# Performance work log

Measured on AMD Instinct MI355X. Metric: run time of the kernel, lower is better.

## Reference

```python
import jax, jax.numpy as jnp
from jax import lax
import numpy as np

B = 64          # batch
HW = 28         # image height/width (hardcoded in module)
LATENT = 256    # latent_size
LABEL = 10      # label_size
FEAT = 64 * HW * HW  # 50176, encoder/decoder fc feature dim


def _conv(x, w, pad):
    # x: [N,C,H,W], w: [O,I,kH,kW]
    return lax.conv_general_dilated(
        x, w, (1, 1), ((pad, pad), (pad, pad)),
        dimension_numbers=('NCHW', 'OIHW', 'NCHW'))


def _conv_transpose(x, w, b, pad):
    # ConvTranspose2d(stride=1, padding=pad) == conv with flipped, transposed
    # kernel and padding k-1-pad. w: [I,O,kH,kW] (torch ConvTranspose layout).
    k = w.shape[2]
    wt = jnp.flip(w, (2, 3)).transpose(1, 0, 2, 3)  # [O,I,kH,kW]
    return _conv(x, wt, k - 1 - pad) + b[None, :, None, None]


def _encoder(images, c1w, c1b, c2w, c2b, fcw, fcb):
    x = jax.nn.relu(_conv(images, c1w, 2) + c1b[None, :, None, None])
    x = jax.nn.relu(_conv(x, c2w, 2) + c2b[None, :, None, None])
    x = x.reshape(x.shape[0], FEAT)
    return jnp.tanh(x @ fcw.T + fcb)


def _decoder(z, fcw, fcb, ct2w, ct2b, ct1w, ct1b):
    x = jnp.arctanh(z)
    x = (x @ fcw.T + fcb).reshape(-1, 64, HW, HW)
    x = jax.nn.relu(_conv_transpose(x, ct2w, ct2b, 2))
    return _conv_transpose(x, ct1w, ct1b, 2)


def _hopfield_weight(patterns):
    # TrainHopfield: Hebbian outer-product sum with mean subtraction,
    # zero diagonal, normalized by number of patterns. One GEMM.
    rho = jnp.mean(patterns)
    t = patterns - rho                      # [L, latent]
    w = t.T @ t                             # [latent, latent]
    w = w - jnp.diag(jnp.diag(w))
    return w / patterns.shape[0]


def _cluster(s0, w):
    # Batched version of: iterate s = sign(w @ s) up to LATENT steps,
    # stopping per-sample when energy -s@w@s stops changing.
    def energy(s):
        return -jnp.einsum('bi,ij,bj->b', s, w, s)

    def step(carry, _):
        s, prev_e, done = carry
        new_s = jnp.sign(s @ w.T)           # w symmetric; per-sample w@s
        e = energy(new_s)
        s_next = jnp.where(done[:, None], s, new_s)
        prev_e_next = jnp.where(done, prev_e, e)
        done_next = done | (e == prev_e)
        return (s_next, prev_e_next, done_next), None

    init = (s0, energy(s0), jnp.zeros(s0.shape[0], dtype=bool))
    (s, _, _), _ = lax.scan(step, init, None, length=LATENT)
    return s


def setup_inputs() -> dict:
    key = jax.random.key(0)
    ks = jax.random.split(key, 12)
    s = 0.05
    f32 = jnp.float32
    return {
        'images': jax.random.normal(ks[0], (B, 1, HW, HW), f32),
        'enc_c1_w': jax.random.normal(ks[1], (32, 1, 5, 5), f32) * s,
        'enc_c1_b': jnp.zeros((32,), f32),
        'enc_c2_w': jax.random.normal(ks[2], (64, 32, 5, 5), f32) * s,
        'enc_c2_b': jnp.zeros((64,), f32),
        'enc_fc_w': jax.random.normal(ks[3], (LATENT, FEAT), f32) * 0.005,
        'enc_fc_b': jnp.zeros((LATENT,), f32),
        'dec_fc_w': jax.random.normal(ks[4], (FEAT, LATENT), f32) * s,
        'dec_fc_b': jnp.zeros((FEAT,), f32),
        'dec_ct2_w': jax.random.normal(ks[5], (64, 32, 5, 5), f32) * s,
        'dec_ct2_b': jnp.zeros((32,), f32),
        'dec_ct1_w': jax.random.normal(ks[6], (32, 1, 5, 5), f32) * s,
        'dec_ct1_b': jnp.zeros((1,), f32),
        'sm_w': jax.random.normal(ks[7], (LABEL, LATENT), f32) * s,
        'sm_b': jnp.zeros((LABEL,), f32),
        'label_latent': jnp.tanh(jax.random.normal(ks[8], (LABEL, LATENT), f32)),
    }


def reference(images, enc_c1_w, enc_c1_b, enc_c2_w, enc_c2_b, enc_fc_w,
              enc_fc_b, dec_fc_w, dec_fc_b, dec_ct2_w, dec_ct2_b, dec_ct1_w,
              dec_ct1_b, sm_w, sm_b, label_latent):
    z = _encoder(images, enc_c1_w, enc_c1_b, enc_c2_w, enc_c2_b,
                 enc_fc_w, enc_fc_b)                       # [B, latent]
    w = _hopfield_weight(jnp.sign(label_latent))           # [latent, latent]
    s0 = lax.stop_gradient(jnp.sign(z))                    # detached copy
    clustered = _cluster(s0, w)                            # [B, latent]
    cluster_probs = jax.nn.softmax(clustered @ label_latent.T, axis=1)
    class_probs = jax.nn.softmax(z @ sm_w.T + sm_b, axis=1)
    recon = _decoder(z, dec_fc_w, dec_fc_b, dec_ct2_w, dec_ct2_b,
                     dec_ct1_w, dec_ct1_b)                 # [B,1,28,28]
    return (cluster_probs, class_probs, recon)
```

## Files before the change

### kernel.cpp

```cpp
#include <hip/hip_runtime.h>
#include <hip/hip_bf16.h>
#include <math.h>

#define BATCH 64
#define HW 28
#define PIX 784
#define LATENT 256
#define LABEL 10
#define FEAT 50176
#define KS 28
#define KCH 1792
#define TSTR 36

typedef __attribute__((ext_vector_type(8))) short bf16x8;
typedef __attribute__((ext_vector_type(4))) float f32x4;

__device__ __forceinline__ float sgnf(float v) {
    return (v > 0.f) ? 1.f : ((v < 0.f) ? -1.f : 0.f);
}

__device__ __forceinline__ short f2bf(float f) {
    union { float f; unsigned u; } v; v.f = f;
    unsigned r = v.u + 0x7FFF + ((v.u >> 16) & 1);
    return (short)(r >> 16);
}
__device__ __forceinline__ float bf2f(short s) {
    union { unsigned u; float f; } v; v.u = ((unsigned)(unsigned short)s) << 16;
    return v.f;
}

template<int G, int FLIP>
__global__ __launch_bounds__(256) void conv5_k(const float* __restrict__ in,
                        const float* __restrict__ w,
                        const float* __restrict__ bias, float* __restrict__ out,
                        int IC, int OC, int relu) {
    int b = blockIdx.x, oc0 = blockIdx.y * G;
    __shared__ float plp[2][32 * TSTR];
    int tid = threadIdx.x;

    for (int t = tid; t < 2 * 32 * TSTR; t += 256) ((float*)plp)[t] = 0.f;

    bool actS = tid < 196;
    int ys = tid / 7, qs = tid % 7;

    int q = tid & 7, yy = tid >> 3;
    bool actC = (q < 7) && (yy < 28);
    int x0 = q * 4;

    float acc[G][4];
    #pragma unroll
    for (int g = 0; g < G; ++g)
        #pragma unroll
        for (int xi = 0; xi < 4; ++xi) acc[g][xi] = 0.f;

    __syncthreads();
    if (actS) {
        float4 v = *(const float4*)&in[((size_t)(b * IC + 0)) * PIX + tid * 4];
        *(float2*)&plp[0][(ys + 2) * TSTR + 4 * qs + 2] = make_float2(v.x, v.y);
        *(float2*)&plp[0][(ys + 2) * TSTR + 4 * qs + 4] = make_float2(v.z, v.w);
    }
    __syncthreads();

    for (int ic = 0; ic < IC; ++ic) {
        float4 vn;
        bool more = (ic + 1) < IC;
        if (more && actS)
            vn = *(const float4*)&in[((size_t)(b * IC + ic + 1)) * PIX + tid * 4];

        const float* tile = plp[ic & 1];
        if (actC) {
            #pragma unroll
            for (int dy = 0; dy < 5; ++dy) {
                float4 ra = *(const float4*)&tile[(yy + dy) * TSTR + x0];
                float4 rb = *(const float4*)&tile[(yy + dy) * TSTR + x0 + 4];
                float rw[8] = {ra.x, ra.y, ra.z, ra.w, rb.x, rb.y, rb.z, rb.w};
                #pragma unroll
                for (int g = 0; g < G; ++g) {
                    #pragma unroll
                    for (int dx = 0; dx < 5; ++dx) {
                        float wv = FLIP
                            ? w[((size_t)ic * OC + (oc0 + g)) * 25 + (4 - dy) * 5 + (4 - dx)]
                            : w[((size_t)(oc0 + g) * IC + ic) * 25 + dy * 5 + dx];
                        #pragma unroll
                        for (int xi = 0; xi < 4; ++xi)
                            acc[g][xi] += rw[xi + dx] * wv;
                    }
                }
            }
        }
        if (more && actS) {
            float* nt = plp[(ic + 1) & 1];
            *(float2*)&nt[(ys + 2) * TSTR + 4 * qs + 2] = make_float2(vn.x, vn.y);
            *(float2*)&nt[(ys + 2) * TSTR + 4 * qs + 4] = make_float2(vn.z, vn.w);
        }
        __syncthreads();
    }

    if (actC) {
        #pragma unroll
        for (int g = 0; g < G; ++g) {
            float bv = bias[oc0 + g];
            float4 o;
            o.x = acc[g][0] + bv;
            o.y = acc[g][1] + bv;
            o.z = acc[g][2] + bv;
            o.w = acc[g][3] + bv;
            if (relu) {
                o.x = fmaxf(o.x, 0.f); o.y = fmaxf(o.y, 0.f);
                o.z = fmaxf(o.z, 0.f); o.w = fmaxf(o.w, 0.f);
            }
            *(float4*)&out[((size_t)(b * OC + (oc0 + g))) * PIX + yy * HW + x0] = o;
        }
    }
}

__global__ __launch_bounds__(64) void c2_mfma_k(const short* __restrict__ xh,
                        const short* __restrict__ xm, const short* __restrict__ xl,
                        const short* __restrict__ wb,
                        const float* __restrict__ bias, float* __restrict__ out) {
    int b = blockIdx.x;
    int t0 = blockIdx.y * 4;
    int lane = threadIdx.x;
    int prow = lane & 15, kgrp = lane >> 4;

    f32x4 acc[4][4];
    #pragma unroll
    for (int pt = 0; pt < 4; ++pt)
        #pragma unroll
        for (int nt = 0; nt < 4; ++nt) acc[pt][nt] = (f32x4){0.f, 0.f, 0.f, 0.f};

    int py[4], px[4];
    bool ptv[4];
    #pragma unroll
    for (int pt = 0; pt < 4; ++pt) {
        int p = (t0 + pt) * 16 + prow;
        ptv[pt] = (t0 + pt) < 49;
        py[pt] = p / 28; px[pt] = p % 28;
    }

    for (int tap = 0; tap < 25; ++tap) {
        int dy = tap / 5 - 2, dx = tap % 5 - 2;
        const short* wt = wb + (size_t)tap * 2048;
        bf16x8 B0[4], B1[4], B2[4];
        #pragma unroll
        for (int nt = 0; nt < 4; ++nt) {
            int off = (nt * 16 + prow) * 32 + kgrp * 8;
            B0[nt] = *(const bf16x8*)&wt[off];
            B1[nt] = *(const bf16x8*)&wt[51200 + off];
            B2[nt] = *(const bf16x8*)&wt[102400 + off];
        }
        #pragma unroll
        for (int pt = 0; pt < 4; ++pt) {
            int ysrc = py[pt] + dy, xsrc = px[pt] + dx;
            bool valid = ptv[pt] && (ysrc >= 0) && (ysrc < 28) && (xsrc >= 0) && (xsrc < 28);
            bf16x8 ah = {0,0,0,0,0,0,0,0}, am = {0,0,0,0,0,0,0,0}, al = {0,0,0,0,0,0,0,0};
            if (valid) {
                size_t o = ((size_t)b * PIX + ysrc * 28 + xsrc) * 32 + kgrp * 8;
                ah = *(const bf16x8*)&xh[o];
                am = *(const bf16x8*)&xm[o];
                al = *(const bf16x8*)&xl[o];
            }
            #pragma unroll
            for (int nt = 0; nt < 4; ++nt) {
                acc[pt][nt] = __builtin_amdgcn_mfma_f32_16x16x32_bf16(ah, B0[nt], acc[pt][nt], 0, 0, 0);
                acc[pt][nt] = __builtin_amdgcn_mfma_f32_16x16x32_bf16(ah, B1[nt], acc[pt][nt], 0, 0, 0);
                acc[pt][nt] = __builtin_amdgcn_mfma_f32_16x16x32_bf16(am, B0[nt], acc[pt][nt], 0, 0, 0);
                acc[pt][nt] = __builtin_amdgcn_mfma_f32_16x16x32_bf16(ah, B2[nt], acc[pt][nt], 0, 0, 0);
                acc[pt][nt] = __builtin_amdgcn_mfma_f32_16x16x32_bf16(am, B1[nt], acc[pt][nt], 0, 0, 0);
                acc[pt][nt] = __builtin_amdgcn_mfma_f32_16x16x32_bf16(al, B0[nt], acc[pt][nt], 0, 0, 0);
            }
        }
    }

    __shared__ float ot[64][17];
    float bv = bias[lane];
    for (int pt = 0; pt < 4; ++pt) {
        if (!ptv[pt]) continue;
        #pragma unroll
        for (int nt = 0; nt < 4; ++nt)
            #pragma unroll
            for (int r = 0; r < 4; ++r)
                ot[nt * 16 + prow][kgrp * 4 + r] = acc[pt][nt][r];
        float* op = &out[((size_t)(b * 64 + lane)) * PIX + (t0 + pt) * 16];
        #pragma unroll
        for (int i = 0; i < 4; ++i) {
            float4 o;
            o.x = fmaxf(ot[lane][i * 4 + 0] + bv, 0.f);
            o.y = fmaxf(ot[lane][i * 4 + 1] + bv, 0.f);
            o.z = fmaxf(ot[lane][i * 4 + 2] + bv, 0.f);
            o.w = fmaxf(ot[lane][i * 4 + 3] + bv, 0.f);
            *(float4*)&op[i * 4] = o;
        }
    }
}

__global__ void xsplit3_k(const float* __restrict__ x, short* __restrict__ xh,
                          short* __restrict__ xm, short* __restrict__ xl) {
    __shared__ float lds[32][17];
    int b = blockIdx.x, pbase = blockIdx.y * 16;
    int t = threadIdx.x;
    if (t < 128) {
        int ic = t >> 2, pj = (t & 3) * 4;
        float4 v = *(const float4*)&x[((size_t)(b * 32 + ic)) * PIX + pbase + pj];
        lds[ic][pj + 0] = v.x; lds[ic][pj + 1] = v.y;
        lds[ic][pj + 2] = v.z; lds[ic][pj + 3] = v.w;
    }
    __syncthreads();
    int p = t >> 4, ic2 = (t & 15) * 2;
    size_t o = ((size_t)b * PIX + pbase + p) * 32 + ic2;
    short2 h, m, l;
    {
        float v = lds[ic2][p];
        short s0 = f2bf(v); float r = v - bf2f(s0);
        short s1 = f2bf(r); float r2 = r - bf2f(s1);
        h.x = s0; m.x = s1; l.x = f2bf(r2);
    }
    {
        float v = lds[ic2 + 1][p];
        short s0 = f2bf(v); float r = v - bf2f(s0);
        short s1 = f2bf(r); float r2 = r - bf2f(s1);
        h.y = s0; m.y = s1; l.y = f2bf(r2);
    }
    *(short2*)&xh[o] = h;
    *(short2*)&xm[o] = m;
    *(short2*)&xl[o] = l;
}

__global__ void wprep3_k(const float* __restrict__ w, short* __restrict__ wb) {
    int j = blockIdx.x * 256 + threadIdx.x;
    if (j < 51200) {
        int ic = j & 31;
        int oc = (j >> 5) & 63;
        int tap = j >> 11;
        float v = w[((size_t)oc * 32 + ic) * 25 + tap];
        short s0 = f2bf(v); float r = v - bf2f(s0);
        short s1 = f2bf(r); float r2 = r - bf2f(s1);
        wb[j] = s0;
        wb[51200 + j] = s1;
        wb[102400 + j] = f2bf(r2);
    }
}

__global__ __launch_bounds__(64) void ct2_mfma_k(const short* __restrict__ xb,
                        const short* __restrict__ wb,
                        const float* __restrict__ bias, float* __restrict__ out) {
    int b = blockIdx.x;
    int pbase = blockIdx.y * 16;
    int lane = threadIdx.x;
    int prow = lane & 15;
    int kgrp = lane >> 4;
    int p = pbase + prow;
    int py = p / 28, px = p % 28;

    f32x4 acc0 = {0.f, 0.f, 0.f, 0.f};
    f32x4 acc1 = {0.f, 0.f, 0.f, 0.f};

    for (int tap = 0; tap < 25; ++tap) {
        int dy = tap / 5 - 2, dx = tap % 5 - 2;
        int ysrc = py + dy, xsrc = px + dx;
        bool valid = (ysrc >= 0) && (ysrc < 28) && (xsrc >= 0) && (xsrc < 28);
        int ps = ysrc * 28 + xsrc;

        bf16x8 a0 = {0,0,0,0,0,0,0,0}, a1 = {0,0,0,0,0,0,0,0};
        if (valid) {
            const bf16x8* ap = (const bf16x8*)&xb[((size_t)b * PIX + ps) * 64 + kgrp * 8];
            a0 = ap[0];
            a1 = ap[4];
        }
        const short* wt = &wb[(size_t)tap * 32 * 64];
        int oc_l = lane & 15;
        bf16x8 b00 = *(const bf16x8*)&wt[oc_l * 64 + kgrp * 8];
        bf16x8 b01 = *(const bf16x8*)&wt[oc_l * 64 + 32 + kgrp * 8];
        bf16x8 b10 = *(const bf16x8*)&wt[(16 + oc_l) * 64 + kgrp * 8];
        bf16x8 b11 = *(const bf16x8*)&wt[(16 + oc_l) * 64 + 32 + kgrp * 8];

        acc0 = __builtin_amdgcn_mfma_f32_16x16x32_bf16(a0, b00, acc0, 0, 0, 0);
        acc0 = __builtin_amdgcn_mfma_f32_16x16x32_bf16(a1, b01, acc0, 0, 0, 0);
        acc1 = __builtin_amdgcn_mfma_f32_16x16x32_bf16(a0, b10, acc1, 0, 0, 0);
        acc1 = __builtin_amdgcn_mfma_f32_16x16x32_bf16(a1, b11, acc1, 0, 0, 0);
    }

    __shared__ float ot[32][16];
    int drow = (lane >> 4) * 4;
    #pragma unroll
    for (int r = 0; r < 4; ++r) {
        ot[lane & 15][drow + r]        = acc0[r];
        ot[16 + (lane & 15)][drow + r] = acc1[r];
    }
    __syncthreads();
    int oc = lane >> 1, ph = (lane & 1) * 8;
    float bv = bias[oc];
    float4 o0, o1;
    o0.x = fmaxf(ot[oc][ph + 0] + bv, 0.f);
    o0.y = fmaxf(ot[oc][ph + 1] + bv, 0.f);
    o0.z = fmaxf(ot[oc][ph + 2] + bv, 0.f);
    o0.w = fmaxf(ot[oc][ph + 3] + bv, 0.f);
    o1.x = fmaxf(ot[oc][ph + 4] + bv, 0.f);
    o1.y = fmaxf(ot[oc][ph + 5] + bv, 0.f);
    o1.z = fmaxf(ot[oc][ph + 6] + bv, 0.f);
    o1.w = fmaxf(ot[oc][ph + 7] + bv, 0.f);
    float* op = &out[((size_t)(b * 32 + oc)) * PIX + pbase + ph];
    *(float4*)&op[0] = o0;
    *(float4*)&op[4] = o1;
}

__global__ void wprep_k(const float* __restrict__ w, short* __restrict__ wb) {
    int j = blockIdx.x * 256 + threadIdx.x;
    if (j < 25 * 32 * 64) {
        int ic = j & 63;
        int oc = (j >> 6) & 31;
        int tap = j >> 11;
        int dyi = tap / 5, dxi = tap % 5;
        wb[j] = f2bf(w[((size_t)ic * 32 + oc) * 25 + (4 - dyi) * 5 + (4 - dxi)]);
    }
}

__global__ void xpose16_k(const short* __restrict__ y16, short* __restrict__ xb) {
    __shared__ short lds[64][16];
    int b = blockIdx.x, pbase = blockIdx.y * 16;
    int t = threadIdx.x;
    {
        int ic = t >> 2, pj = (t & 3) * 4;
        short4 v = *(const short4*)&y16[((size_t)(b * 64 + ic)) * PIX + pbase + pj];
        lds[ic][pj + 0] = v.x;
        lds[ic][pj + 1] = v.y;
        lds[ic][pj + 2] = v.z;
        lds[ic][pj + 3] = v.w;
    }
    __syncthreads();
    {
        int p = t >> 4, icq = (t & 15) * 4;
        short4 s;
        s.x = lds[icq + 0][p];
        s.y = lds[icq + 1][p];
        s.z = lds[icq + 2][p];
        s.w = lds[icq + 3][p];
        *(short4*)&xb[((size_t)b * PIX + pbase + p) * 64 + icq] = s;
    }
}

__global__ void enc_fc_part_k(const float* __restrict__ x, const float* __restrict__ w,
                              float* __restrict__ part) {
    int n0 = blockIdx.x * 4;
    int ks = blockIdx.y;
    int kl = threadIdx.x & 31;
    int mi = threadIdx.x >> 5;

    float acc[8][4];
    #pragma unroll
    for (int mg = 0; mg < 8; ++mg)
        #pragma unroll
        for (int nt = 0; nt < 4; ++nt) acc[mg][nt] = 0.f;

    int kend = (ks + 1) * KCH;
    for (int kk = ks * KCH + kl * 4; kk < kend; kk += 128) {
        float4 xv[8];
        #pragma unroll
        for (int mg = 0; mg < 8; ++mg)
            xv[mg] = *(const float4*)&x[(size_t)(mg * 8 + mi) * FEAT + kk];
        #pragma unroll
        for (int nt = 0; nt < 4; ++nt) {
            float4 wv = *(const float4*)&w[(size_t)(n0 + nt) * FEAT + kk];
            #pragma unroll
            for (int mg = 0; mg < 8; ++mg) {
                acc[mg][nt] += xv[mg].x * wv.x + xv[mg].y * wv.y
                             + xv[mg].z * wv.z + xv[mg].w * wv.w;
            }
        }
    }

    #pragma unroll
    for (int mg = 0; mg < 8; ++mg) {
        #pragma unroll
        for (int nt = 0; nt < 4; ++nt) {
            float v = acc[mg][nt];
            v += __shfl_xor(v, 16, 64);
            v += __shfl_xor(v, 8, 64);
            v += __shfl_xor(v, 4, 64);
            v += __shfl_xor(v, 2, 64);
            v += __shfl_xor(v, 1, 64);
            if (kl == 0)
                part[(ks * BATCH + (mg * 8 + mi)) * LATENT + (n0 + nt)] = v;
        }
    }
}

__global__ void enc_fc_fin_k(const float* __restrict__ part, const float* __restrict__ bias,
                             float* __restrict__ z, short* __restrict__ xah,
                             short* __restrict__ xam) {
    int m = blockIdx.x;
    int n = threadIdx.x;
    int idx = m * 256 + n;
    float a = bias[n];
    for (int ksi = 0; ksi < KS; ++ksi) a += part[ksi * BATCH * LATENT + idx];
    float zv = tanhf(a);
    z[idx] = zv;
    float xv = atanhf(zv);
    short h = f2bf(xv);
    xah[idx] = h;
    xam[idx] = f2bf(xv - bf2f(h));
}

__global__ void hop_rho_k(const float* __restrict__ ll, float* __restrict__ rho_out) {
    float p = 0.f;
    for (int t = threadIdx.x; t < LABEL * LATENT; t += 256) p += sgnf(ll[t]);
    __shared__ float red[8];
    for (int o = 32; o; o >>= 1) p += __shfl_down(p, o, 64);
    if ((threadIdx.x & 63) == 0) red[threadIdx.x >> 6] = p;
    __syncthreads();
    if (threadIdx.x == 0)
        rho_out[0] = (red[0] + red[1] + red[2] + red[3]) / (float)(LABEL * LATENT);
}

__global__ void hop_w_k(const float* __restrict__ ll, const float* __restrict__ rho_p,
                        float* __restrict__ wout) {
    int i = blockIdx.x, j = threadIdx.x;
    float rho = rho_p[0];
    float acc = 0.f;
    #pragma unroll
    for (int l = 0; l < LABEL; ++l) {
        float a = sgnf(ll[l * LATENT + i]) - rho;
        float b = sgnf(ll[l * LATENT + j]) - rho;
        acc += a * b;
    }
    wout[i * LATENT + j] = (i == j) ? 0.f : acc / 10.f;
}

__global__ __launch_bounds__(1024) void cluster_k(const float* __restrict__ z,
                          const float* __restrict__ w,
                          const float* __restrict__ ll, float* __restrict__ out) {
    int b = blockIdx.x;
    int t = threadIdx.x;
    int i = t & 255;
    int q = t >> 8;
    int lane = t & 63;
    int wvid = t >> 6;

    __shared__ float s_sh[LATENT];
    __shared__ float part[1024];
    __shared__ float red[4];
    __shared__ float cflag[4];
    __shared__ int ctl_sh;
    __shared__ float logit[LABEL];

    float wreg[64];
    #pragma unroll
    for (int jj = 0; jj < 64; ++jj)
        wreg[jj] = w[(q * 64 + jj) * LATENT + i];

    float s_cur = 0.f, s_old = 2.f, v = 0.f;
    float e_prev = 0.f;
    if (q == 0) {
        s_cur = sgnf(z[b * LATENT + i]);
        s_sh[i] = s_cur;
    }
    __syncthreads();

    {
        float p0 = 0.f, p1 = 0.f;
        #pragma unroll
        for (int jj = 0; jj < 64; jj += 2) {
            p0 += wreg[jj]     * s_sh[q * 64 + jj];
            p1 += wreg[jj + 1] * s_sh[q * 64 + jj + 1];
        }
        part[t] = p0 + p1;
    }
    __syncthreads();
    if (q == 0) {
        v = part[i] + part[i + 256] + part[i + 512] + part[i + 768];
        float p = s_cur * v;
        #pragma unroll
        for (int o = 32; o; o >>= 1) p += __shfl_down(p, o, 64);
        if (lane == 0) red[wvid] = p;
    }
    __syncthreads();
    if (t == 0) e_prev = -(red[0] + red[1] + red[2] + red[3]);

    for (int it = 0; it < LATENT; ++it) {
        if (q == 0) {
            float ns = sgnf(v);
            unsigned long long m = __ballot(ns == s_old);
            if (lane == 0) cflag[wvid] = (m == ~0ull) ? 1.f : 0.f;
            s_sh[i] = ns;
            s_old = s_cur;
            s_cur = ns;
        }
        __syncthreads();
        {
            float p0 = 0.f, p1 = 0.f;
            #pragma unroll
            for (int jj = 0; jj < 64; jj += 2) {
                p0 += wreg[jj]     * s_sh[q * 64 + jj];
                p1 += wreg[jj + 1] * s_sh[q * 64 + jj + 1];
            }
            part[t] = p0 + p1;
        }
        __syncthreads();
        if (q == 0) {
            v = part[i] + part[i + 256] + part[i + 512] + part[i + 768];
            float p = s_cur * v;
            #pragma unroll
            for (int o = 32; o; o >>= 1) p += __shfl_down(p, o, 64);
            if (lane == 0) red[wvid] = p;
        }
        __syncthreads();
        if (t == 0) {
            float e = -(red[0] + red[1] + red[2] + red[3]);
            int c = 0;
            if (e == e_prev) c = 1;
            else if (it >= 1 && cflag[0] != 0.f && cflag[1] != 0.f &&
                     cflag[2] != 0.f && cflag[3] != 0.f)
                c = (((LATENT - 1 - it) & 1) == 0) ? 2 : 3;
            else e_prev = e;
            ctl_sh = c;
        }
        __syncthreads();
        int c = ctl_sh;
        if (c != 0) {
            if (c == 3 && q == 0) s_sh[i] = s_old;
            break;
        }
    }
    __syncthreads();

    if (wvid < LABEL) {
        float p = 0.f;
        #pragma unroll
        for (int r = 0; r < 4; ++r)
            p += s_sh[r * 64 + lane] * ll[wvid * LATENT + r * 64 + lane];
        #pragma unroll
        for (int o = 32; o; o >>= 1) p += __shfl_down(p, o, 64);
        if (lane == 0) logit[wvid] = p;
    }
    __syncthreads();
    if (t == 0) {
        float mx = logit[0];
        for (int c = 1; c < LABEL; ++c) mx = fmaxf(mx, logit[c]);
        float ex[LABEL];
        float s = 0.f;
        for (int c = 0; c < LABEL; ++c) { ex[c] = expf(logit[c] - mx); s += ex[c]; }
        for (int c = 0; c < LABEL; ++c) out[b * LABEL + c] = ex[c] / s;
    }
}

__device__ __forceinline__ float block_sum256(float p, float* red) {
    __syncthreads();
    for (int o = 32; o; o >>= 1) p += __shfl_down(p, o, 64);
    if ((threadIdx.x & 63) == 0) red[threadIdx.x >> 6] = p;
    __syncthreads();
    return red[0] + red[1] + red[2] + red[3];
}

__global__ void class_k(const float* __restrict__ z, const float* __restrict__ smw,
                        const float* __restrict__ smb, float* __restrict__ out) {
    int b = blockIdx.x;
    int i = threadIdx.x;
    __shared__ float red[8];
    __shared__ float logit[LABEL];
    float zi = z[b * LATENT + i];
    for (int c = 0; c < LABEL; ++c) {
        float p = zi * smw[c * LATENT + i];
        float t = block_sum256(p, red);
        if (i == 0) logit[c] = t + smb[c];
    }
    __syncthreads();
    if (i == 0) {
        float mx = logit[0];
        for (int c = 1; c < LABEL; ++c) mx = fmaxf(mx, logit[c]);
        float ex[LABEL];
        float s = 0.f;
        for (int c = 0; c < LABEL; ++c) { ex[c] = expf(logit[c] - mx); s += ex[c]; }
        for (int c = 0; c < LABEL; ++c) out[b * LABEL + c] = ex[c] / s;
    }
}

__global__ __launch_bounds__(256) void dec_fc_mfma_k(const short* __restrict__ xah,
                         const short* __restrict__ xam,
                         const float* __restrict__ w,
                         const float* __restrict__ bias, short* __restrict__ y16) {
    int tid = threadIdx.x;
    int lane = tid & 63, wv = tid >> 6;
    int prow = lane & 15, kgrp = lane >> 4;
    int n0 = blockIdx.x * 64;
    int nb = n0 + wv * 16;

    f32x4 acc[4];
    #pragma unroll
    for (int mi = 0; mi < 4; ++mi) acc[mi] = (f32x4){0.f, 0.f, 0.f, 0.f};

    for (int kc = 0; kc < 8; ++kc) {
        int kof = kc * 32 + kgrp * 8;
        const float* wp = &w[(size_t)(nb + prow) * LATENT + kof];
        float4 w0 = *(const float4*)&wp[0];
        float4 w1 = *(const float4*)&wp[4];
        bf16x8 bf;
        bf[0] = f2bf(w0.x); bf[1] = f2bf(w0.y); bf[2] = f2bf(w0.z); bf[3] = f2bf(w0.w);
        bf[4] = f2bf(w1.x); bf[5] = f2bf(w1.y); bf[6] = f2bf(w1.z); bf[7] = f2bf(w1.w);
        #pragma unroll
        for (int mi = 0; mi < 4; ++mi) {
            bf16x8 ah = *(const bf16x8*)&xah[(mi * 16 + prow) * LATENT + kof];
            bf16x8 am = *(const bf16x8*)&xam[(mi * 16 + prow) * LATENT + kof];
            acc[mi] = __builtin_amdgcn_mfma_f32_16x16x32_bf16(ah, bf, acc[mi], 0, 0, 0);
            acc[mi] = __builtin_amdgcn_mfma_f32_16x16x32_bf16(am, bf, acc[mi], 0, 0, 0);
        }
    }

    __shared__ short ot[64 * 72];
    float bv = bias[nb + prow];
    #pragma unroll
    for (int mi = 0; mi < 4; ++mi)
        #pragma unroll
        for (int r = 0; r < 4; ++r) {
            int m = mi * 16 + kgrp * 4 + r;
            ot[m * 72 + wv * 16 + prow] = f2bf(acc[mi][r] + bv);
        }
    __syncthreads();
    int m = tid >> 2, q = tid & 3;
    #pragma unroll
    for (int i = 0; i < 2; ++i) {
        *(int4*)&y16[(size_t)m * FEAT + n0 + i * 32 + q * 8] =
            *(int4*)&ot[m * 72 + i * 32 + q * 8];
    }
}

extern "C" void kernel_launch(void* const* d_in, const int* in_sizes, int n_in,
                              void* d_out, int out_size, void* d_ws, size_t ws_size,
                              hipStream_t stream) {
    const float* images   = (const float*)d_in[0];
    const float* c1w      = (const float*)d_in[1];
    const float* c1b      = (const float*)d_in[2];
    const float* c2w      = (const float*)d_in[3];
    const float* c2b      = (const float*)d_in[4];
    const float* efw      = (const float*)d_in[5];
    const float* efb      = (const float*)d_in[6];
    const float* dfw      = (const float*)d_in[7];
    const float* dfb      = (const float*)d_in[8];
    const float* ct2w     = (const float*)d_in[9];
    const float* ct2b     = (const float*)d_in[10];
    const float* ct1w     = (const float*)d_in[11];
    const float* ct1b     = (const float*)d_in[12];
    const float* smw      = (const float*)d_in[13];
    const float* smb      = (const float*)d_in[14];
    const float* ll       = (const float*)d_in[15];

    float* out = (float*)d_out;
    float* ws  = (float*)d_ws;

    float* big0 = ws;
    float* big1 = ws + 3211264;
    float* part = ws + 3211264 + 1605632;
    float* z    = part + KS * BATCH * LATENT;
    float* whop = z + BATCH * LATENT;
    float* rho  = whop + LATENT * LATENT;
    float* xsa  = rho + 4;
    short* xah  = (short*)xsa;
    short* xam  = xah + 16384;
    short* xbf  = (short*)(xsa + 16384);
    short* wbf  = (short*)(xsa + 16384 + 1605632);
    short* xh3  = xbf;
    short* xm3  = xbf + 1605632;
    short* xl3  = (short*)(xsa + 16384 + 1605632 + 25600);
    short* wb3  = xl3 + 1605632;
    short* y16  = (short*)big0;

    conv5_k<4,0><<<dim3(BATCH, 8), 256, 0, stream>>>(images, c1w, c1b, big1, 1, 32, 1);
    wprep3_k<<<200, 256, 0, stream>>>(c2w, wb3);
    xsplit3_k<<<dim3(BATCH, 49), 256, 0, stream>>>(big1, xh3, xm3, xl3);
    c2_mfma_k<<<dim3(BATCH, 13), 64, 0, stream>>>(xh3, xm3, xl3, wb3, c2b, big0);
    enc_fc_part_k<<<dim3(64, KS), 256, 0, stream>>>(big0, efw, part);
    enc_fc_fin_k<<<BATCH, 256, 0, stream>>>(part, efb, z, xah, xam);

    hop_rho_k<<<1, 256, 0, stream>>>(ll, rho);
    hop_w_k<<<LATENT, 256, 0, stream>>>(ll, rho, whop);
    cluster_k<<<BATCH, 1024, 0, stream>>>(z, whop, ll, out);
    class_k<<<BATCH, 256, 0, stream>>>(z, smw, smb, out + 640);

    wprep_k<<<200, 256, 0, stream>>>(ct2w, wbf);
    dec_fc_mfma_k<<<FEAT / 64, 256, 0, stream>>>(xah, xam, dfw, dfb, y16);
    xpose16_k<<<dim3(BATCH, 49), 256, 0, stream>>>(y16, xbf);
    ct2_mfma_k<<<dim3(BATCH, 49), 64, 0, stream>>>(xbf, wbf, ct2b, big1);
    conv5_k<1,1><<<dim3(BATCH, 1), 256, 0, stream>>>(big1, ct1w, ct1b, out + 1280, 32, 1, 0);
}
```

Measured before the change: 295.9 us.

## Move encoder FC to split-bf16 MFMA with wider K split-reduction

Replaces the scalar FP32 encoder fully-connected kernel with an MFMA kernel. Each block handles a 512-wide K slice for all 64x256 outputs. Operands are split on the fly into three bf16 parts and combined with six MFMAs to keep near-FP32 accuracy. The K split grows from 28 to 98 partial slices, with the partial buffer moved to reuse the bf16 workspace. This trades scalar FMA throughput for matrix-core throughput, at the cost of extra split arithmetic, a larger partial-sum reduction in the finalize kernel, and 64KB of LDS per block.

```diff
diff --git a/kernel.cpp b/kernel.cpp
--- a/kernel.cpp
+++ b/kernel.cpp
@@ -8,8 +8,7 @@
 #define LATENT 256
 #define LABEL 10
 #define FEAT 50176
-#define KS 28
-#define KCH 1792
+#define KS 98
 #define TSTR 36
 
 typedef __attribute__((ext_vector_type(8))) short bf16x8;
@@ -27,6 +26,19 @@
 __device__ __forceinline__ float bf2f(short s) {
     union { unsigned u; float f; } v; v.u = ((unsigned)(unsigned short)s) << 16;
     return v.f;
+}
+
+__device__ __forceinline__ void split3(const float* __restrict__ p,
+                                       bf16x8& h, bf16x8& m, bf16x8& l) {
+    float4 a = *(const float4*)p;
+    float4 b = *(const float4*)(p + 4);
+    float v[8] = {a.x, a.y, a.z, a.w, b.x, b.y, b.z, b.w};
+    #pragma unroll
+    for (int j = 0; j < 8; ++j) {
+        short s0 = f2bf(v[j]); float r = v[j] - bf2f(s0);
+        short s1 = f2bf(r);    float r2 = r - bf2f(s1);
+        h[j] = s0; m[j] = s1; l[j] = f2bf(r2);
+    }
 }
 
 template<int G, int FLIP>
@@ -339,49 +351,60 @@
     }
 }
 
-__global__ void enc_fc_part_k(const float* __restrict__ x, const float* __restrict__ w,
-                              float* __restrict__ part) {
-    int n0 = blockIdx.x * 4;
-    int ks = blockIdx.y;
-    int kl = threadIdx.x & 31;
-    int mi = threadIdx.x >> 5;
-
-    float acc[8][4];
-    #pragma unroll
-    for (int mg = 0; mg < 8; ++mg)
-        #pragma unroll
-        for (int nt = 0; nt < 4; ++nt) acc[mg][nt] = 0.f;
-
-    int kend = (ks + 1) * KCH;
-    for (int kk = ks * KCH + kl * 4; kk < kend; kk += 128) {
-        float4 xv[8];
-        #pragma unroll
-        for (int mg = 0; mg < 8; ++mg)
-            xv[mg] = *(const float4*)&x[(size_t)(mg * 8 + mi) * FEAT + kk];
-        #pragma unroll
-        for (int nt = 0; nt < 4; ++nt) {
-            float4 wv = *(const float4*)&w[(size_t)(n0 + nt) * FEAT + kk];
+__global__ __launch_bounds__(512) void enc_fc_mfma_k(const float* __restrict__ x,
+                        const float* __restrict__ w, float* __restrict__ part) {
+    int ks = blockIdx.x;
+    int kbase = ks * 512;
+    int tid = threadIdx.x;
+    int lane = tid & 63, wv = tid >> 6;
+    int prow = lane & 15, kgrp = lane >> 4;
+
+    f32x4 acc[4][2];
+    #pragma unroll
+    for (int mt = 0; mt < 4; ++mt)
+        #pragma unroll
+        for (int ntl = 0; ntl < 2; ++ntl) acc[mt][ntl] = (f32x4){0.f, 0.f, 0.f, 0.f};
+
+    for (int kt = 0; kt < 16; ++kt) {
+        int kof = kbase + kt * 32 + kgrp * 8;
+        bf16x8 ah[4], am[4], al[4];
+        #pragma unroll
+        for (int mt = 0; mt < 4; ++mt)
+            split3(&x[(size_t)(mt * 16 + prow) * FEAT + kof], ah[mt], am[mt], al[mt]);
+        #pragma unroll
+        for (int ntl = 0; ntl < 2; ++ntl) {
+            bf16x8 bh, bm, bl;
+            split3(&w[(size_t)(wv * 32 + ntl * 16 + prow) * FEAT + kof], bh, bm, bl);
             #pragma unroll
-            for (int mg = 0; mg < 8; ++mg) {
-                acc[mg][nt] += xv[mg].x * wv.x + xv[mg].y * wv.y
-                             + xv[mg].z * wv.z + xv[mg].w * wv.w;
+            for (int mt = 0; mt < 4; ++mt) {
+                acc[mt][ntl] = __builtin_amdgcn_mfma_f32_16x16x32_bf16(ah[mt], bh, acc[mt][ntl], 0, 0, 0);
+                acc[mt][ntl] = __builtin_amdgcn_mfma_f32_16x16x32_bf16(ah[mt], bm, acc[mt][ntl], 0, 0, 0);
+                acc[mt][ntl] = __builtin_amdgcn_mfma_f32_16x16x32_bf16(am[mt], bh, acc[mt][ntl], 0, 0, 0);
+                acc[mt][ntl] = __builtin_amdgcn_mfma_f32_16x16x32_bf16(ah[mt], bl, acc[mt][ntl], 0, 0, 0);
+                acc[mt][ntl] = __builtin_amdgcn_mfma_f32_16x16x32_bf16(am[mt], bm, acc[mt][ntl], 0, 0, 0);
+                acc[mt][ntl] = __builtin_amdgcn_mfma_f32_16x16x32_bf16(al[mt], bh, acc[mt][ntl], 0, 0, 0);
             }
         }
     }
 
-    #pragma unroll
-    for (int mg = 0; mg < 8; ++mg) {
-        #pragma unroll
-        for (int nt = 0; nt < 4; ++nt) {
-            float v = acc[mg][nt];
-            v += __shfl_xor(v, 16, 64);
-            v += __shfl_xor(v, 8, 64);
-            v += __shfl_xor(v, 4, 64);
-            v += __shfl_xor(v, 2, 64);
-            v += __shfl_xor(v, 1, 64);
-            if (kl == 0)
-                part[(ks * BATCH + (mg * 8 + mi)) * LATENT + (n0 + nt)] = v;
-        }
+    __shared__ float ot[64 * 257];
+    #pragma unroll
+    for (int mt = 0; mt < 4; ++mt)
+        #pragma unroll
+        for (int ntl = 0; ntl < 2; ++ntl)
+            #pragma unroll
+            for (int r = 0; r < 4; ++r) {
+                int m = mt * 16 + kgrp * 4 + r;
+                int n = wv * 32 + ntl * 16 + prow;
+                ot[m * 257 + n] = acc[mt][ntl][r];
+            }
+    __syncthreads();
+    int m = tid >> 3, c0 = (tid & 7) * 4;
+    float* pp = &part[(size_t)ks * BATCH * LATENT + m * 256];
+    #pragma unroll
+    for (int i = 0; i < 8; ++i) {
+        int n = c0 + i * 32;
+        *(float4*)&pp[n] = *(float4*)&ot[m * 257 + n];
     }
 }
 
@@ -392,7 +415,7 @@
     int n = threadIdx.x;
     int idx = m * 256 + n;
     float a = bias[n];
-    for (int ksi = 0; ksi < KS; ++ksi) a += part[ksi * BATCH * LATENT + idx];
+    for (int ksi = 0; ksi < KS; ++ksi) a += part[(size_t)ksi * BATCH * LATENT + idx];
     float zv = tanhf(a);
     z[idx] = zv;
     float xv = atanhf(zv);
@@ -648,8 +671,7 @@
 
     float* big0 = ws;
     float* big1 = ws + 3211264;
-    float* part = ws + 3211264 + 1605632;
-    float* z    = part + KS * BATCH * LATENT;
+    float* z    = ws + 3211264 + 1605632 + 458752;
     float* whop = z + BATCH * LATENT;
     float* rho  = whop + LATENT * LATENT;
     float* xsa  = rho + 4;
@@ -662,12 +684,13 @@
     short* xl3  = (short*)(xsa + 16384 + 1605632 + 25600);
     short* wb3  = xl3 + 1605632;
     short* y16  = (short*)big0;
+    float* part = (float*)xbf;
 
     conv5_k<4,0><<<dim3(BATCH, 8), 256, 0, stream>>>(images, c1w, c1b, big1, 1, 32, 1);
     wprep3_k<<<200, 256, 0, stream>>>(c2w, wb3);
     xsplit3_k<<<dim3(BATCH, 49), 256, 0, stream>>>(big1, xh3, xm3, xl3);
     c2_mfma_k<<<dim3(BATCH, 13), 64, 0, stream>>>(xh3, xm3, xl3, wb3, c2b, big0);
-    enc_fc_part_k<<<dim3(64, KS), 256, 0, stream>>>(big0, efw, part);
+    enc_fc_mfma_k<<<KS, 512, 0, stream>>>(big0, efw, part);
     enc_fc_fin_k<<<BATCH, 256, 0, stream>>>(part, efb, z, xah, xam);
 
     hop_rho_k<<<1, 256, 0, stream>>>(ll, rho);
```

After: 296.5 us. About the same (+0.2%).
